# Kernel tuning notes

Hardware: AMD Instinct MI355X
Metric: run time of the kernel (lower is better)

## Reference

```python
import jax, jax.numpy as jnp
import numpy as np

N_HEAD, N_KV_HEAD, N_EMBD, SEQ_LEN = 16, 4, 1024, 2048
HEAD_DIM = N_EMBD // N_HEAD  # 64
B = 2


def _rope(x, cos, sin):
    # x: [B, T, H, D]; cos/sin: [1, T, 1, D//2]
    d = x.shape[-1] // 2
    x1, x2 = x[..., :d], x[..., d:]
    return jnp.concatenate([x1 * cos + x2 * sin, -x1 * sin + x2 * cos], axis=-1)


def setup_inputs() -> dict:
    key = jax.random.key(0)
    ks = jax.random.split(key, 5)
    x = jax.random.normal(ks[0], (B, SEQ_LEN, N_EMBD), dtype=jnp.float32)
    # real RoPE tables (base 10000)
    half = HEAD_DIM // 2
    inv_freq = 1.0 / (10000.0 ** (jnp.arange(half, dtype=jnp.float32) / half))
    ang = jnp.arange(SEQ_LEN, dtype=jnp.float32)[:, None] * inv_freq[None, :]  # [T, half]
    cos = jnp.cos(ang)[None, :, None, :]  # [1, T, 1, half]
    sin = jnp.sin(ang)[None, :, None, :]
    s = 0.02
    Wq = s * jax.random.normal(ks[1], (N_EMBD, N_HEAD * HEAD_DIM), dtype=jnp.float32)
    Wk = s * jax.random.normal(ks[2], (N_EMBD, N_KV_HEAD * HEAD_DIM), dtype=jnp.float32)
    Wv = s * jax.random.normal(ks[3], (N_EMBD, N_KV_HEAD * HEAD_DIM), dtype=jnp.float32)
    Wo = s * jax.random.normal(ks[4], (N_EMBD, N_EMBD), dtype=jnp.float32)
    return {"x": x, "cos": cos, "sin": sin, "Wq": Wq, "Wk": Wk, "Wv": Wv, "Wo": Wo}


def reference(x, cos, sin, Wq, Wk, Wv, Wo):
    Bsz, T, C = x.shape
    H, Hkv, D = N_HEAD, N_KV_HEAD, HEAD_DIM
    q = (x @ Wq).reshape(Bsz, T, H, D)
    k = (x @ Wk).reshape(Bsz, T, Hkv, D)
    v = (x @ Wv).reshape(Bsz, T, Hkv, D)
    q = _rope(q, cos, sin)
    k = _rope(k, cos, sin)
    # GQA: repeat kv heads to match query heads
    rep = H // Hkv
    k = jnp.repeat(k, rep, axis=2)  # [B, T, H, D]
    v = jnp.repeat(v, rep, axis=2)
    scale = 1.0 / np.sqrt(D).astype(np.float32)
    att = jnp.einsum('bqhd,bkhd->bhqk', q, k) * scale  # [B, H, T, T]
    causal = jnp.tril(jnp.ones((T, T), dtype=bool))
    att = jnp.where(causal[None, None, :, :], att, -jnp.inf)
    att = jax.nn.softmax(att, axis=-1)
    y = jnp.einsum('bhqk,bkhd->bqhd', att, v).reshape(Bsz, T, C)
    return y @ Wo
```

## Files before the change

### kernel.cpp

```cpp
#include <hip/hip_runtime.h>
#include <hip/hip_bf16.h>


typedef __attribute__((ext_vector_type(8))) short s16x8;
typedef __attribute__((ext_vector_type(4))) float f32x4;
typedef __attribute__((ext_vector_type(4))) unsigned short u16x4;

#define LOG2E 1.44269504088896340736f

__device__ __forceinline__ float bf2f(unsigned short u) {
  unsigned int i = ((unsigned int)u) << 16;
  return __builtin_bit_cast(float, i);
}
__device__ __forceinline__ unsigned short f2bf(float f) {
  unsigned int i = __builtin_bit_cast(unsigned int, f);
  i += 0x7fffu + ((i >> 16) & 1u);
  return (unsigned short)(i >> 16);
}

__device__ __forceinline__ void async16(const void* g, void* l) {
  __builtin_amdgcn_global_load_lds(
      (const __attribute__((address_space(1))) void*)g,
      (__attribute__((address_space(3))) void*)l, 16, 0, 0);
}


__global__ void conv_f32_to_bf16(const float* __restrict__ in,
                                 unsigned short* __restrict__ out, int n) {
  int i = (blockIdx.x * blockDim.x + threadIdx.x) * 4;
  if (i + 3 < n) {
    float4 v = *(const float4*)(in + i);
    u16x4 o = { f2bf(v.x), f2bf(v.y), f2bf(v.z), f2bf(v.w) };
    *(u16x4*)(out + i) = o;
  }
}

__global__ void transpose_conv4(const float* __restrict__ W0,
                                const float* __restrict__ W1,
                                const float* __restrict__ W2,
                                const float* __restrict__ W3,
                                unsigned short* __restrict__ D0,
                                unsigned short* __restrict__ D1,
                                unsigned short* __restrict__ D2,
                                unsigned short* __restrict__ D3) {
  __shared__ float tile[32][33];
  int z = blockIdx.z;
  const float* W = (z == 0) ? W0 : (z == 1) ? W1 : (z == 2) ? W2 : W3;
  unsigned short* Wt = (z == 0) ? D0 : (z == 1) ? D1 : (z == 2) ? D2 : D3;
  int N = (z == 1 || z == 2) ? 256 : 1024;
  const int K = 1024;
  int n0 = blockIdx.x * 32, k0 = blockIdx.y * 32;
  if (n0 >= N) return;
  int tx = threadIdx.x, ty = threadIdx.y;
  for (int i = ty; i < 32; i += 8)
    tile[i][tx] = W[(size_t)(k0 + i) * N + n0 + tx];
  __syncthreads();
  for (int i = ty; i < 32; i += 8)
    Wt[(size_t)(n0 + i) * K + k0 + tx] = f2bf(tile[tx][i]);
}

__global__ void rope_qk(unsigned short* __restrict__ QKV,
                        const float* __restrict__ cosb,
                        const float* __restrict__ sinb) {
  int idx = blockIdx.x * blockDim.x + threadIdx.x;
  int d = idx & 31;
  int hh = (idx >> 5) % 20;
  int row = idx / (32 * 20);
  int t = row & 2047;
  size_t base;
  float mul;
  if (hh < 16) { base = (size_t)row * 1536 + hh * 64 + d;               mul = 0.125f; }
  else         { base = (size_t)row * 1536 + 1024 + (hh - 16) * 64 + d; mul = 1.0f;   }
  float x1 = bf2f(QKV[base]), x2 = bf2f(QKV[base + 32]);
  float c = cosb[t * 32 + d], s = sinb[t * 32 + d];
  QKV[base]      = f2bf((x1 * c + x2 * s) * mul);
  QKV[base + 32] = f2bf((-x1 * s + x2 * c) * mul);
}

__global__ __launch_bounds__(256) void gemm_bt(
    const unsigned short* __restrict__ A, const unsigned short* __restrict__ Bt,
    void* __restrict__ Cp, int M, int N, int K, int c_f32) {
  __shared__ unsigned short As[128 * 64];
  __shared__ unsigned short Bs[64 * 64];
  int tid = threadIdx.x;
  int w = tid >> 6, l = tid & 63, g = l >> 4, lr = l & 15;
  int wr = w >> 1, wc = w & 1;

  int nb = gridDim.x, bid = blockIdx.x;
  int wg = (bid & 7) * (nb >> 3) + (bid >> 3);
  int nx = N >> 6;
  int m0 = (wg / nx) * 128, n0 = (wg % nx) * 64;
  int sk = lr & 7;

  f32x4 acc[4][2] = {};

  for (int k0 = 0; k0 < K; k0 += 64) {
#pragma unroll
    for (int i = 0; i < 4; ++i) {
      int c = i * 256 + tid;
      int row = c >> 3, srcu = ((c & 7) ^ (row & 7)) * 8;
      async16(A + (size_t)(m0 + row) * K + k0 + srcu, (char*)As + c * 16);
    }
#pragma unroll
    for (int i = 0; i < 2; ++i) {
      int c = i * 256 + tid;
      int row = c >> 3, srcu = ((c & 7) ^ (row & 7)) * 8;
      async16(Bt + (size_t)(n0 + row) * K + k0 + srcu, (char*)Bs + c * 16);
    }
    __syncthreads();

    s16x8 af[2][4], bfr[2][2];
#pragma unroll
    for (int ks = 0; ks < 2; ++ks) {
#pragma unroll
      for (int m = 0; m < 4; ++m)
        af[ks][m] = *(const s16x8*)(As + (wr * 64 + m * 16 + lr) * 64 +
                                    ((ks * 4 + g) ^ sk) * 8);
#pragma unroll
      for (int n = 0; n < 2; ++n)
        bfr[ks][n] = *(const s16x8*)(Bs + (wc * 32 + n * 16 + lr) * 64 +
                                     ((ks * 4 + g) ^ sk) * 8);
    }
#pragma unroll
    for (int ks = 0; ks < 2; ++ks)
#pragma unroll
      for (int m = 0; m < 4; ++m)
#pragma unroll
        for (int n = 0; n < 2; ++n)
          acc[m][n] = __builtin_amdgcn_mfma_f32_16x16x32_bf16(
              af[ks][m], bfr[ks][n], acc[m][n], 0, 0, 0);
    __syncthreads();
  }

  if (c_f32) {
    float* C = (float*)Cp;
#pragma unroll
    for (int m = 0; m < 4; ++m)
#pragma unroll
      for (int n = 0; n < 2; ++n)
#pragma unroll
        for (int r = 0; r < 4; ++r)
          C[(size_t)(m0 + wr * 64 + m * 16 + g * 4 + r) * N +
            n0 + wc * 32 + n * 16 + lr] = acc[m][n][r];
  } else {
    unsigned short* C = (unsigned short*)Cp;
#pragma unroll
    for (int m = 0; m < 4; ++m)
#pragma unroll
      for (int n = 0; n < 2; ++n)
#pragma unroll
        for (int r = 0; r < 4; ++r)
          C[(size_t)(m0 + wr * 64 + m * 16 + g * 4 + r) * N +
            n0 + wc * 32 + n * 16 + lr] = f2bf(acc[m][n][r]);
  }
}

__global__ __launch_bounds__(256) void attn_fused(
    const unsigned short* __restrict__ QKV, unsigned short* __restrict__ Y) {
  __shared__ unsigned short Kt[2][64 * 64];
  __shared__ unsigned short Vt[2][64 * 64];
  __shared__ unsigned short Pb[4][16 * 64];

  const int T = 2048, CS = 1536;
  int tid = threadIdx.x;
  int w = tid >> 6, l = tid & 63, g = l >> 4, lr = l & 15;
  int n = blockIdx.x;
  int ip = n >> 5;
  int bh = n & 31, b = bh >> 4, h = bh & 15, kvh = h >> 2;
  int sx = lr & 7;

  const unsigned short* Qp = QKV + (size_t)b * T * CS + h * 64;
  const unsigned short* Kp = QKV + (size_t)b * T * CS + 1024 + kvh * 64;
  const unsigned short* Vp = QKV + (size_t)b * T * CS + 1280 + kvh * 64;
  unsigned short* Pw = Pb[w];

  int kvA = tid & 63, dA = (tid >> 6) * 8, dB = dA + 32;

  for (int pass = 0; pass < 2; ++pass) {
    int qt = pass == 0 ? (31 - ip) : ip;
    int qw = qt * 64 + w * 16;
    int q_mine = qw + lr;

    s16x8 qf[2];
#pragma unroll
    for (int ks = 0; ks < 2; ++ks)
      qf[ks] = *(const s16x8*)(Qp + (size_t)q_mine * CS + ks * 32 + g * 8);

    f32x4 o[4] = {};
    float mrun = -1e30f, lrun = 0.f;
    int ntiles = qt + 1;

#pragma unroll
    for (int i = 0; i < 2; ++i) {
      int c = i * 256 + tid;
      int row = c >> 3, srcc = ((c & 7) ^ (row & 7)) * 8;
      async16(Kp + (size_t)row * CS + srcc, (char*)(&Kt[0][0]) + c * 16);
    }
#pragma unroll
    for (int i = 0; i < 2; ++i) {
      int c = i * 256 + tid;
      int kv = c & 63, d0v = (c >> 6) * 8;
      s16x8 vv = *(const s16x8*)(Vp + (size_t)kv * CS + d0v);
#pragma unroll
      for (int j = 0; j < 8; ++j)
        Vt[0][(d0v + j) * 64 + (kv ^ (j * 8))] = (unsigned short)vv[j];
    }
    __syncthreads();

    int cur = 0;
    for (int it = 0; it < ntiles; ++it) {
      int kv0 = it * 64;
      bool hasnext = (it + 1 < ntiles);

      s16x8 vvA, vvB;
      if (hasnext) {
        int kvn = kv0 + 64;
#pragma unroll
        for (int i = 0; i < 2; ++i) {
          int c = i * 256 + tid;
          int row = c >> 3, srcc = ((c & 7) ^ (row & 7)) * 8;
          async16(Kp + (size_t)(kvn + row) * CS + srcc,
                  (char*)(&Kt[cur ^ 1][0]) + c * 16);
        }
        vvA = *(const s16x8*)(Vp + (size_t)(kvn + kvA) * CS + dA);
        vvB = *(const s16x8*)(Vp + (size_t)(kvn + kvA) * CS + dB);
      }

      const unsigned short* Kc = &Kt[cur][0];
      const unsigned short* Vc = &Vt[cur][0];
      f32x4 s[4];
      __builtin_amdgcn_s_setprio(1);
#pragma unroll
      for (int nf = 0; nf < 4; ++nf) {
        f32x4 z = {};
#pragma unroll
        for (int ks = 0; ks < 2; ++ks) {
          s16x8 kf = *(const s16x8*)(Kc + (nf * 16 + lr) * 64 +
                                     ((ks * 4 + g) ^ sx) * 8);
          z = __builtin_amdgcn_mfma_f32_16x16x32_bf16(kf, qf[ks], z, 0, 0, 0);
        }
        s[nf] = z;
      }
      __builtin_amdgcn_s_setprio(0);

      if (it == ntiles - 1) {
#pragma unroll
        for (int nf = 0; nf < 4; ++nf)
#pragma unroll
          for (int r = 0; r < 4; ++r)
            if (kv0 + nf * 16 + g * 4 + r > q_mine) s[nf][r] = -1e30f;
      }

      float mt = s[0][0];
#pragma unroll
      for (int nf = 0; nf < 4; ++nf)
#pragma unroll
        for (int r = 0; r < 4; ++r) mt = fmaxf(mt, s[nf][r]);
      mt = fmaxf(mt, __shfl_xor(mt, 16, 64));
      mt = fmaxf(mt, __shfl_xor(mt, 32, 64));

      if (__any(mt > mrun + 8.f)) {
        float mnew = fmaxf(mrun, mt);
        float corr = exp2f((mrun - mnew) * LOG2E);
        float psum = 0.f;
#pragma unroll
        for (int nf = 0; nf < 4; ++nf)
#pragma unroll
          for (int r = 0; r < 4; ++r) {
            float p = exp2f((s[nf][r] - mnew) * LOG2E);
            s[nf][r] = p;
            psum += p;
          }
        psum += __shfl_xor(psum, 16, 64);
        psum += __shfl_xor(psum, 32, 64);
        lrun = lrun * corr + psum;
        mrun = mnew;
#pragma unroll
        for (int r = 0; r < 4; ++r) {
          float cr = __shfl(corr, g * 4 + r, 64);
#pragma unroll
          for (int d0 = 0; d0 < 4; ++d0) o[d0][r] *= cr;
        }
      } else {
        float psum = 0.f;
#pragma unroll
        for (int nf = 0; nf < 4; ++nf)
#pragma unroll
          for (int r = 0; r < 4; ++r) {
            float p = exp2f((s[nf][r] - mrun) * LOG2E);
            s[nf][r] = p;
            psum += p;
          }
        psum += __shfl_xor(psum, 16, 64);
        psum += __shfl_xor(psum, 32, 64);
        lrun += psum;
      }

#pragma unroll
      for (int nf = 0; nf < 4; ++nf) {
        u16x4 pv = { f2bf(s[nf][0]), f2bf(s[nf][1]),
                     f2bf(s[nf][2]), f2bf(s[nf][3]) };
        *(u16x4*)(Pw + lr * 64 + ((nf * 16 + g * 4) ^ (sx * 8))) = pv;
      }
      asm volatile("s_waitcnt lgkmcnt(0)" ::: "memory");
      __builtin_amdgcn_sched_barrier(0);

      s16x8 pf[2];
#pragma unroll
      for (int ks = 0; ks < 2; ++ks)
        pf[ks] = *(const s16x8*)(Pw + lr * 64 + ((ks * 4 + g) ^ sx) * 8);
      __builtin_amdgcn_s_setprio(1);
#pragma unroll
      for (int d0 = 0; d0 < 4; ++d0)
#pragma unroll
        for (int ks = 0; ks < 2; ++ks) {
          s16x8 vf = *(const s16x8*)(Vc + (d0 * 16 + lr) * 64 +
                                     ((ks * 4 + g) ^ sx) * 8);
          o[d0] = __builtin_amdgcn_mfma_f32_16x16x32_bf16(pf[ks], vf, o[d0], 0, 0, 0);
        }
      __builtin_amdgcn_s_setprio(0);

      if (hasnext) {
#pragma unroll
        for (int j = 0; j < 8; ++j)
          Vt[cur ^ 1][(dA + j) * 64 + (kvA ^ (j * 8))] = (unsigned short)vvA[j];
#pragma unroll
        for (int j = 0; j < 8; ++j)
          Vt[cur ^ 1][(dB + j) * 64 + (kvA ^ (j * 8))] = (unsigned short)vvB[j];
      }
      __syncthreads();
      cur ^= 1;
    }

#pragma unroll
    for (int r = 0; r < 4; ++r) {
      float lv = __shfl(lrun, g * 4 + r, 64);
      float inv = 1.f / lv;
      size_t rowoff = (size_t)(b * T + qw + g * 4 + r) * 1024 + h * 64;
#pragma unroll
      for (int d0 = 0; d0 < 4; ++d0)
        Y[rowoff + d0 * 16 + lr] = f2bf(o[d0][r] * inv);
    }
  }
}


extern "C" void kernel_launch(void* const* d_in, const int* in_sizes, int n_in,
                              void* d_out, int out_size, void* d_ws, size_t ws_size,
                              hipStream_t stream) {
  const float* x    = (const float*)d_in[0];
  const float* cosb = (const float*)d_in[1];
  const float* sinb = (const float*)d_in[2];
  const float* Wq   = (const float*)d_in[3];
  const float* Wk   = (const float*)d_in[4];
  const float* Wv   = (const float*)d_in[5];
  const float* Wo   = (const float*)d_in[6];
  float* out = (float*)d_out;

  char* ob = (char*)d_out;
  char* ws = (char*)d_ws;
  const size_t MB = 1024 * 1024;
  unsigned short* QKVb  = (unsigned short*)(ob);
  unsigned short* xb    = (unsigned short*)(ws);
  unsigned short* Wqkvt = (unsigned short*)(ws + 8 * MB);
  unsigned short* Wot   = (unsigned short*)(ws + 11 * MB);
  unsigned short* Yb    = xb;

  conv_f32_to_bf16<<<4096, 256, 0, stream>>>(x, xb, 4096 * 1024);
  transpose_conv4<<<dim3(32, 32, 4), dim3(32, 8), 0, stream>>>(
      Wq, Wk, Wv, Wo,
      Wqkvt, Wqkvt + (size_t)1024 * 1024, Wqkvt + (size_t)1280 * 1024, Wot);

  gemm_bt<<<dim3(768), 256, 0, stream>>>(xb, Wqkvt, QKVb, 4096, 1536, 1024, 0);

  rope_qk<<<10240, 256, 0, stream>>>(QKVb, cosb, sinb);

  attn_fused<<<dim3(512), 256, 0, stream>>>(QKVb, Yb);

  gemm_bt<<<dim3(512), 256, 0, stream>>>(Yb, Wot, out, 4096, 1024, 1024, 1);
}
```

Measured before the change: 125.6 us.

## Fuse Q RoPE and log2e scaling into attention; vectorize V transpose stores

Applies RoPE to Q inside the attention kernel while loading Q fragments, folding the 1/sqrt(D) scale and log2e into Q so the softmax can call exp2 without extra multiplies. The separate rope kernel now handles only K heads, which cuts its grid and its read-modify-write traffic over the Q columns. V tiles are transposed into LDS with 4x4 register blocks and 8-byte stores instead of scalar 2-byte stores. The patch also uses a packed bf16 conversion instruction for P and Q, and splits the max and sum reductions into independent chains. The cos/sin tables are now re-read per query row in attention, and the rescale threshold is adjusted to the log2 domain.

```diff
diff --git a/kernel.cpp b/kernel.cpp
--- a/kernel.cpp
+++ b/kernel.cpp
@@ -5,6 +5,7 @@
 typedef __attribute__((ext_vector_type(8))) short s16x8;
 typedef __attribute__((ext_vector_type(4))) float f32x4;
 typedef __attribute__((ext_vector_type(4))) unsigned short u16x4;
+typedef __attribute__((ext_vector_type(4))) unsigned int u32x4;
 
 #define LOG2E 1.44269504088896340736f
 
@@ -16,6 +17,11 @@
   unsigned int i = __builtin_bit_cast(unsigned int, f);
   i += 0x7fffu + ((i >> 16) & 1u);
   return (unsigned short)(i >> 16);
+}
+__device__ __forceinline__ unsigned int cvtpk(float lo, float hi) {
+  unsigned int r;
+  asm("v_cvt_pk_bf16_f32 %0, %1, %2" : "=v"(r) : "v"(lo), "v"(hi));
+  return r;
 }
 
 __device__ __forceinline__ void async16(const void* g, void* l) {
@@ -59,22 +65,19 @@
     Wt[(size_t)(n0 + i) * K + k0 + tx] = f2bf(tile[tx][i]);
 }
 
-__global__ void rope_qk(unsigned short* __restrict__ QKV,
-                        const float* __restrict__ cosb,
-                        const float* __restrict__ sinb) {
+__global__ void rope_k(unsigned short* __restrict__ QKV,
+                       const float* __restrict__ cosb,
+                       const float* __restrict__ sinb) {
   int idx = blockIdx.x * blockDim.x + threadIdx.x;
   int d = idx & 31;
-  int hh = (idx >> 5) % 20;
-  int row = idx / (32 * 20);
+  int hk = (idx >> 5) & 3;
+  int row = idx >> 7;
   int t = row & 2047;
-  size_t base;
-  float mul;
-  if (hh < 16) { base = (size_t)row * 1536 + hh * 64 + d;               mul = 0.125f; }
-  else         { base = (size_t)row * 1536 + 1024 + (hh - 16) * 64 + d; mul = 1.0f;   }
+  size_t base = (size_t)row * 1536 + 1024 + hk * 64 + d;
   float x1 = bf2f(QKV[base]), x2 = bf2f(QKV[base + 32]);
   float c = cosb[t * 32 + d], s = sinb[t * 32 + d];
-  QKV[base]      = f2bf((x1 * c + x2 * s) * mul);
-  QKV[base + 32] = f2bf((-x1 * s + x2 * c) * mul);
+  QKV[base]      = f2bf(x1 * c + x2 * s);
+  QKV[base + 32] = f2bf(-x1 * s + x2 * c);
 }
 
 __global__ __launch_bounds__(256) void gemm_bt(
@@ -156,7 +159,8 @@
 }
 
 __global__ __launch_bounds__(256) void attn_fused(
-    const unsigned short* __restrict__ QKV, unsigned short* __restrict__ Y) {
+    const unsigned short* __restrict__ QKV, unsigned short* __restrict__ Y,
+    const float* __restrict__ cosb, const float* __restrict__ sinb) {
   __shared__ unsigned short Kt[2][64 * 64];
   __shared__ unsigned short Vt[2][64 * 64];
   __shared__ unsigned short Pb[4][16 * 64];
@@ -174,7 +178,8 @@
   const unsigned short* Vp = QKV + (size_t)b * T * CS + 1280 + kvh * 64;
   unsigned short* Pw = Pb[w];
 
-  int kvA = tid & 63, dA = (tid >> 6) * 8, dB = dA + 32;
+  int kvg = (tid & 15) * 4, dcc = (tid >> 4) * 4;
+  int vcol0 = kvg ^ ((dcc & 7) * 8);
 
   for (int pass = 0; pass < 2; ++pass) {
     int qt = pass == 0 ? (31 - ip) : ip;
@@ -182,9 +187,30 @@
     int q_mine = qw + lr;
 
     s16x8 qf[2];
-#pragma unroll
-    for (int ks = 0; ks < 2; ++ks)
-      qf[ks] = *(const s16x8*)(Qp + (size_t)q_mine * CS + ks * 32 + g * 8);
+    {
+      s16x8 q0 = *(const s16x8*)(Qp + (size_t)q_mine * CS + g * 8);
+      s16x8 q1 = *(const s16x8*)(Qp + (size_t)q_mine * CS + 32 + g * 8);
+      float cc[8], ss[8];
+      *(float4*)(cc) = *(const float4*)(cosb + q_mine * 32 + g * 8);
+      *(float4*)(cc + 4) = *(const float4*)(cosb + q_mine * 32 + g * 8 + 4);
+      *(float4*)(ss) = *(const float4*)(sinb + q_mine * 32 + g * 8);
+      *(float4*)(ss + 4) = *(const float4*)(sinb + q_mine * 32 + g * 8 + 4);
+      const float SC = 0.125f * LOG2E;
+      float y1[8], y2[8];
+#pragma unroll
+      for (int j = 0; j < 8; ++j) {
+        float x1 = bf2f((unsigned short)q0[j]);
+        float x2 = bf2f((unsigned short)q1[j]);
+        y1[j] = (x1 * cc[j] + x2 * ss[j]) * SC;
+        y2[j] = (x2 * cc[j] - x1 * ss[j]) * SC;
+      }
+      u32x4 p0 = { cvtpk(y1[0], y1[1]), cvtpk(y1[2], y1[3]),
+                   cvtpk(y1[4], y1[5]), cvtpk(y1[6], y1[7]) };
+      u32x4 p1 = { cvtpk(y2[0], y2[1]), cvtpk(y2[2], y2[3]),
+                   cvtpk(y2[4], y2[5]), cvtpk(y2[6], y2[7]) };
+      qf[0] = __builtin_bit_cast(s16x8, p0);
+      qf[1] = __builtin_bit_cast(s16x8, p1);
+    }
 
     f32x4 o[4] = {};
     float mrun = -1e30f, lrun = 0.f;
@@ -196,14 +222,17 @@
       int row = c >> 3, srcc = ((c & 7) ^ (row & 7)) * 8;
       async16(Kp + (size_t)row * CS + srcc, (char*)(&Kt[0][0]) + c * 16);
     }
-#pragma unroll
-    for (int i = 0; i < 2; ++i) {
-      int c = i * 256 + tid;
-      int kv = c & 63, d0v = (c >> 6) * 8;
-      s16x8 vv = *(const s16x8*)(Vp + (size_t)kv * CS + d0v);
-#pragma unroll
-      for (int j = 0; j < 8; ++j)
-        Vt[0][(d0v + j) * 64 + (kv ^ (j * 8))] = (unsigned short)vv[j];
+    {
+      u16x4 vq[4];
+#pragma unroll
+      for (int k = 0; k < 4; ++k)
+        vq[k] = *(const u16x4*)(Vp + (size_t)(kvg + k) * CS + dcc);
+#pragma unroll
+      for (int j = 0; j < 4; ++j) {
+        u16x4 pk = { (unsigned short)vq[0][j], (unsigned short)vq[1][j],
+                     (unsigned short)vq[2][j], (unsigned short)vq[3][j] };
+        *(u16x4*)(&Vt[0][0] + (dcc + j) * 64 + (vcol0 ^ (j * 8))) = pk;
+      }
     }
     __syncthreads();
 
@@ -212,7 +241,7 @@
       int kv0 = it * 64;
       bool hasnext = (it + 1 < ntiles);
 
-      s16x8 vvA, vvB;
+      u16x4 vq[4];
       if (hasnext) {
         int kvn = kv0 + 64;
 #pragma unroll
@@ -222,8 +251,9 @@
           async16(Kp + (size_t)(kvn + row) * CS + srcc,
                   (char*)(&Kt[cur ^ 1][0]) + c * 16);
         }
-        vvA = *(const s16x8*)(Vp + (size_t)(kvn + kvA) * CS + dA);
-        vvB = *(const s16x8*)(Vp + (size_t)(kvn + kvA) * CS + dB);
+#pragma unroll
+        for (int k = 0; k < 4; ++k)
+          vq[k] = *(const u16x4*)(Vp + (size_t)(kvn + kvg + k) * CS + dcc);
       }
 
       const unsigned short* Kc = &Kt[cur][0];
@@ -251,26 +281,28 @@
             if (kv0 + nf * 16 + g * 4 + r > q_mine) s[nf][r] = -1e30f;
       }
 
-      float mt = s[0][0];
-#pragma unroll
-      for (int nf = 0; nf < 4; ++nf)
-#pragma unroll
-        for (int r = 0; r < 4; ++r) mt = fmaxf(mt, s[nf][r]);
+      float ma = fmaxf(s[0][0], s[1][0]), mb = fmaxf(s[0][1], s[1][1]);
+      float mc = fmaxf(s[0][2], s[1][2]), md = fmaxf(s[0][3], s[1][3]);
+      ma = fmaxf(ma, fmaxf(s[2][0], s[3][0]));
+      mb = fmaxf(mb, fmaxf(s[2][1], s[3][1]));
+      mc = fmaxf(mc, fmaxf(s[2][2], s[3][2]));
+      md = fmaxf(md, fmaxf(s[2][3], s[3][3]));
+      float mt = fmaxf(fmaxf(ma, mb), fmaxf(mc, md));
       mt = fmaxf(mt, __shfl_xor(mt, 16, 64));
       mt = fmaxf(mt, __shfl_xor(mt, 32, 64));
 
-      if (__any(mt > mrun + 8.f)) {
+      if (__any(mt > mrun + 11.5416f)) {
         float mnew = fmaxf(mrun, mt);
-        float corr = exp2f((mrun - mnew) * LOG2E);
-        float psum = 0.f;
-#pragma unroll
-        for (int nf = 0; nf < 4; ++nf)
-#pragma unroll
-          for (int r = 0; r < 4; ++r) {
-            float p = exp2f((s[nf][r] - mnew) * LOG2E);
-            s[nf][r] = p;
-            psum += p;
-          }
+        float corr = exp2f(mrun - mnew);
+        float pa = 0.f, pb = 0.f, pc = 0.f, pd = 0.f;
+#pragma unroll
+        for (int nf = 0; nf < 4; ++nf) {
+          float p0 = exp2f(s[nf][0] - mnew); s[nf][0] = p0; pa += p0;
+          float p1 = exp2f(s[nf][1] - mnew); s[nf][1] = p1; pb += p1;
+          float p2 = exp2f(s[nf][2] - mnew); s[nf][2] = p2; pc += p2;
+          float p3 = exp2f(s[nf][3] - mnew); s[nf][3] = p3; pd += p3;
+        }
+        float psum = (pa + pb) + (pc + pd);
         psum += __shfl_xor(psum, 16, 64);
         psum += __shfl_xor(psum, 32, 64);
         lrun = lrun * corr + psum;
@@ -282,15 +314,15 @@
           for (int d0 = 0; d0 < 4; ++d0) o[d0][r] *= cr;
         }
       } else {
-        float psum = 0.f;
-#pragma unroll
-        for (int nf = 0; nf < 4; ++nf)
-#pragma unroll
-          for (int r = 0; r < 4; ++r) {
-            float p = exp2f((s[nf][r] - mrun) * LOG2E);
-            s[nf][r] = p;
-            psum += p;
-          }
+        float pa = 0.f, pb = 0.f, pc = 0.f, pd = 0.f;
+#pragma unroll
+        for (int nf = 0; nf < 4; ++nf) {
+          float p0 = exp2f(s[nf][0] - mrun); s[nf][0] = p0; pa += p0;
+          float p1 = exp2f(s[nf][1] - mrun); s[nf][1] = p1; pb += p1;
+          float p2 = exp2f(s[nf][2] - mrun); s[nf][2] = p2; pc += p2;
+          float p3 = exp2f(s[nf][3] - mrun); s[nf][3] = p3; pd += p3;
+        }
+        float psum = (pa + pb) + (pc + pd);
         psum += __shfl_xor(psum, 16, 64);
         psum += __shfl_xor(psum, 32, 64);
         lrun += psum;
@@ -298,9 +330,10 @@
 
 #pragma unroll
       for (int nf = 0; nf < 4; ++nf) {
-        u16x4 pv = { f2bf(s[nf][0]), f2bf(s[nf][1]),
-                     f2bf(s[nf][2]), f2bf(s[nf][3]) };
-        *(u16x4*)(Pw + lr * 64 + ((nf * 16 + g * 4) ^ (sx * 8))) = pv;
+        uint2 pv;
+        pv.x = cvtpk(s[nf][0], s[nf][1]);
+        pv.y = cvtpk(s[nf][2], s[nf][3]);
+        *(uint2*)(Pw + lr * 64 + ((nf * 16 + g * 4) ^ (sx * 8))) = pv;
       }
       asm volatile("s_waitcnt lgkmcnt(0)" ::: "memory");
       __builtin_amdgcn_sched_barrier(0);
@@ -321,12 +354,13 @@
       __builtin_amdgcn_s_setprio(0);
 
       if (hasnext) {
-#pragma unroll
-        for (int j = 0; j < 8; ++j)
-          Vt[cur ^ 1][(dA + j) * 64 + (kvA ^ (j * 8))] = (unsigned short)vvA[j];
-#pragma unroll
-        for (int j = 0; j < 8; ++j)
-          Vt[cur ^ 1][(dB + j) * 64 + (kvA ^ (j * 8))] = (unsigned short)vvB[j];
+        unsigned short* Vn = &Vt[cur ^ 1][0];
+#pragma unroll
+        for (int j = 0; j < 4; ++j) {
+          u16x4 pk = { (unsigned short)vq[0][j], (unsigned short)vq[1][j],
+                       (unsigned short)vq[2][j], (unsigned short)vq[3][j] };
+          *(u16x4*)(Vn + (dcc + j) * 64 + (vcol0 ^ (j * 8))) = pk;
+        }
       }
       __syncthreads();
       cur ^= 1;
@@ -373,9 +407,9 @@
 
   gemm_bt<<<dim3(768), 256, 0, stream>>>(xb, Wqkvt, QKVb, 4096, 1536, 1024, 0);
 
-  rope_qk<<<10240, 256, 0, stream>>>(QKVb, cosb, sinb);
-
-  attn_fused<<<dim3(512), 256, 0, stream>>>(QKVb, Yb);
+  rope_k<<<2048, 256, 0, stream>>>(QKVb, cosb, sinb);
+
+  attn_fused<<<dim3(512), 256, 0, stream>>>(QKVb, Yb, cosb, sinb);
 
   gemm_bt<<<dim3(512), 256, 0, stream>>>(Yb, Wot, out, 4096, 1024, 1024, 1);
 }
```

New measurement: 127.3 us. About the same (+1.3%).
